# Performance work log

Hardware: AMD Instinct MI355X
Metric: run time of the kernel (lower is better)

## Reference

```python
import jax, jax.numpy as jnp
import numpy as np

B = 131072   # batch of state samples
H = 512      # hidden width of reconstructed subnets
EPS_DIAG = 0.1  # diagonal regularization ensuring M is invertible


def setup_inputs() -> dict:
    key = jax.random.key(0)
    ks = jax.random.split(key, 20)
    f32 = jnp.float32
    inp = {
        "q":      jax.random.normal(ks[0], (B, 3), dtype=f32),
        "q_dot":  jax.random.normal(ks[1], (B, 3), dtype=f32),
        "s":      jax.random.normal(ks[2], (B, 3), dtype=f32),
        "s_Ddot": jax.random.normal(ks[3], (B, 3), dtype=f32),
        "tau":    jax.random.normal(ks[4], (B, 3), dtype=f32),
        # viscous / coulomb friction coefficients (f_v1..3, f_c1..3)
        "fv": jnp.full((3,), 0.05, dtype=f32),
        "fc": jnp.full((3,), 0.05, dtype=f32),
        # Mass net: 3 -> H -> 9
        "W1m": jax.random.normal(ks[5], (3, H), dtype=f32) * 0.1,
        "b1m": jnp.zeros((H,), dtype=f32),
        "W2m": jax.random.normal(ks[6], (H, 9), dtype=f32) * 0.05,
        "b2m": jnp.zeros((9,), dtype=f32),
        # Gravity net: 3 -> H -> 3
        "W1g": jax.random.normal(ks[7], (3, H), dtype=f32) * 0.1,
        "b1g": jnp.zeros((H,), dtype=f32),
        "W2g": jax.random.normal(ks[8], (H, 3), dtype=f32) * 0.05,
        "b2g": jnp.zeros((3,), dtype=f32),
        # KAB net: concat(q, s, s_Ddot)=9 -> H -> 3
        "W1k": jax.random.normal(ks[9], (9, H), dtype=f32) * 0.1,
        "b1k": jnp.zeros((H,), dtype=f32),
        "W2k": jax.random.normal(ks[10], (H, 3), dtype=f32) * 0.05,
        "b2k": jnp.zeros((3,), dtype=f32),
    }
    return inp


def reference(q, q_dot, s, s_Ddot, tau, fv, fc,
              W1m, b1m, W2m, b2m,
              W1g, b1g, W2g, b2g,
              W1k, b1k, W2k, b2k) -> jnp.ndarray:
    # Mass matrix net -> [B,3,3], made SPD-ish so inv(M) is well defined
    hm = jnp.tanh(q @ W1m + b1m)                       # [B,H]
    Mraw = (hm @ W2m + b2m).reshape(-1, 3, 3)          # [B,3,3]
    M = jnp.einsum('bij,bkj->bik', Mraw, Mraw) + EPS_DIAG * jnp.eye(3, dtype=q.dtype)

    # Gravity net -> [B,3]
    hg = jnp.tanh(q @ W1g + b1g)
    G = hg @ W2g + b2g

    # KAB net on concat(q, s, s_Ddot) -> [B,3]
    x = jnp.concatenate([q, s, s_Ddot], axis=-1)       # [B,9]
    hk = jnp.tanh(x @ W1k + b1k)
    KAB = hk @ W2k + b2k

    # diag(fv) @ q_dot and diag(fc) @ sign(q_dot) are elementwise scalings
    rhs = -G + KAB - fv * q_dot - fc * jnp.sign(q_dot) + tau  # [B,3]

    # q_Ddot = inv(M) @ rhs  (solve is the same math, fewer ops)
    q_Ddot = jnp.linalg.solve(M, rhs[..., None]).squeeze(-1)  # [B,3]
    return q_Ddot
```

## Files before the change

kernel.cpp:

```cpp
#include <hip/hip_runtime.h>
#include <hip/hip_fp16.h>
#include <math.h>

#define HDIM 512
#define NCH1 96
#define NCH2 48
#define EPS_DIAG 0.1f

typedef __fp16 h2 __attribute__((ext_vector_type(2)));
typedef __fp16 h8 __attribute__((ext_vector_type(8)));
typedef float f32x4 __attribute__((ext_vector_type(4)));

__device__ __forceinline__ h2 f2h2(float a, float b) {
    return __builtin_amdgcn_cvt_pkrtz(a, b);
}

__device__ __forceinline__ h2 tanh2(h2 x) {
    const h2 HI = {(__fp16)2.0f,        (__fp16)2.0f};
    const h2 LO = {(__fp16)-2.0f,       (__fp16)-2.0f};
    const h2 C0 = {(__fp16)0.993654f,   (__fp16)0.993654f};
    const h2 C1 = {(__fp16)-0.29463f,   (__fp16)-0.29463f};
    const h2 C2 = {(__fp16)0.0695331f,  (__fp16)0.0695331f};
    const h2 C3 = {(__fp16)-0.00696328f,(__fp16)-0.00696328f};
    h2 t = __builtin_elementwise_min(__builtin_elementwise_max(x, LO), HI);
    h2 u = t * t;
    h2 p = __builtin_elementwise_fma(C3, u, C2);
    p = __builtin_elementwise_fma(p, u, C1);
    p = __builtin_elementwise_fma(p, u, C0);
    return t * p;
}

__global__ void pack_frags(const float* __restrict__ W1m, const float* __restrict__ b1m,
                           const float* __restrict__ W2m,
                           const float* __restrict__ W1g, const float* __restrict__ b1g,
                           const float* __restrict__ W2g,
                           const float* __restrict__ W1k, const float* __restrict__ b1k,
                           const float* __restrict__ W2k,
                           __fp16* __restrict__ frag)
{
    const int tid = blockIdx.x * blockDim.x + threadIdx.x;
    if (tid >= (NCH1 + NCH2) * 64) return;
    const int c = tid >> 6, l = tid & 63;
    __fp16* dst = frag + (size_t)tid * 8;
    if (c < NCH1) {
        const int h = c * 16 + (l & 15);
        #pragma unroll
        for (int j = 0; j < 8; ++j) {
            const int k = (l >> 4) * 8 + j;
            float v = 0.f;
            if (h < 512) {
                if (k < 3) v = W1m[k*HDIM + h];
                else if (k == 9) v = b1m[h];
            } else if (h < 1024) {
                const int hh = h - 512;
                if (k < 3) v = W1g[k*HDIM + hh];
                else if (k == 9) v = b1g[hh];
            } else {
                const int hh = h - 1024;
                if (k < 9) v = W1k[k*HDIM + hh];
                else if (k == 9) v = b1k[hh];
            }
            dst[j] = (__fp16)v;
        }
    } else {
        const int t = c - NCH1;
        const int nOut = l & 15;
        #pragma unroll
        for (int j = 0; j < 8; ++j) {
            const int kp = (l >> 4) * 8 + j;
            const int hid = t*32 + ((kp & 1) << 4) + (kp >> 1);
            float v = 0.f;
            if (hid < 512)       { if (nOut < 9)                v = W2m[hid*9 + nOut]; }
            else if (hid < 1024) { if (nOut >= 9 && nOut < 12)  v = W2g[(hid-512)*3 + (nOut-9)]; }
            else                 { if (nOut >= 12 && nOut < 15) v = W2k[(hid-1024)*3 + (nOut-12)]; }
            dst[j] = (__fp16)v;
        }
    }
}

__global__ __launch_bounds__(256, 6) void dyn_kernel(
    const __fp16* __restrict__ frag,
    const float* __restrict__ q, const float* __restrict__ q_dot,
    const float* __restrict__ s, const float* __restrict__ s_Ddot,
    const float* __restrict__ tau,
    const float* __restrict__ fv, const float* __restrict__ fc,
    const float* __restrict__ b2m, const float* __restrict__ b2g,
    const float* __restrict__ b2k,
    float* __restrict__ out, int n)
{
    __shared__ unsigned int tbuf[4][16][20];
    __shared__ float ebuf[4][16][17];

    const int lane = threadIdx.x & 63;
    const int w    = threadIdx.x >> 6;
    const int col  = lane & 15;
    const int quad = lane >> 4;
    const int base16 = (blockIdx.x * 4 + w) * 16;

    int sm = base16 + col; if (sm >= n) sm = n - 1;
    const float q0 = q[3*sm+0], q1 = q[3*sm+1], q2 = q[3*sm+2];
    const float s0 = s[3*sm+0], s1 = s[3*sm+1], s2 = s[3*sm+2];
    const float d0 = s_Ddot[3*sm+0], d1 = s_Ddot[3*sm+1], d2 = s_Ddot[3*sm+2];
    const bool z0 = (quad == 0), z1 = (quad == 1);
    h8 ax;
    ax[0] = (__fp16)(z0 ? q0 : (z1 ? d2  : 0.f));
    ax[1] = (__fp16)(z0 ? q1 : (z1 ? 1.f : 0.f));
    ax[2] = (__fp16)(z0 ? q2 : 0.f);
    ax[3] = (__fp16)(z0 ? s0 : 0.f);
    ax[4] = (__fp16)(z0 ? s1 : 0.f);
    ax[5] = (__fp16)(z0 ? s2 : 0.f);
    ax[6] = (__fp16)(z0 ? d0 : 0.f);
    ax[7] = (__fp16)(z0 ? d1 : 0.f);

    const f32x4 zero4 = {0.f, 0.f, 0.f, 0.f};
    f32x4 acc = zero4;

    const h8* fw1 = (const h8*)frag + lane;
    const h8* fw2 = (const h8*)frag + (size_t)NCH1 * 64 + lane;

    h8 w1a = fw1[0], w1b = fw1[64], w2v = fw2[0];
    for (int t = 0; t < NCH2; ++t) {
        h8 nw1a, nw1b, nw2;
        const int tn = t + 1;
        if (tn < NCH2) {
            nw1a = fw1[(2*tn    ) * 64];
            nw1b = fw1[(2*tn + 1) * 64];
            nw2  = fw2[tn * 64];
        }
        f32x4 p0 = __builtin_amdgcn_mfma_f32_16x16x32_f16(ax, w1a, zero4, 0, 0, 0);
        f32x4 p1 = __builtin_amdgcn_mfma_f32_16x16x32_f16(ax, w1b, zero4, 0, 0, 0);
        #pragma unroll
        for (int r = 0; r < 4; ++r) {
            const h2 hv = tanh2(f2h2(p0[r], p1[r]));
            tbuf[w][quad*4 + r][col] = __builtin_bit_cast(unsigned int, hv);
        }
        asm volatile("s_waitcnt lgkmcnt(0)" ::: "memory");
        const h8 a2 = *(const h8*)&tbuf[w][col][quad * 4];
        acc = __builtin_amdgcn_mfma_f32_16x16x32_f16(a2, w2v, acc, 0, 0, 0);
        asm volatile("" ::: "memory");
        w1a = nw1a; w1b = nw1b; w2v = nw2;
    }

    #pragma unroll
    for (int r = 0; r < 4; ++r)
        ebuf[w][quad*4 + r][col] = acc[r];
    asm volatile("s_waitcnt lgkmcnt(0)" ::: "memory");

    if (lane < 16) {
        const int i = base16 + lane;
        if (i < n) {
            const float* R = ebuf[w][lane];
            const float bM0 = R[0]  + b2m[0], bM1 = R[1]  + b2m[1], bM2 = R[2]  + b2m[2];
            const float bM3 = R[3]  + b2m[3], bM4 = R[4]  + b2m[4], bM5 = R[5]  + b2m[5];
            const float bM6 = R[6]  + b2m[6], bM7 = R[7]  + b2m[7], bM8 = R[8]  + b2m[8];
            const float bG0 = R[9]  + b2g[0], bG1 = R[10] + b2g[1], bG2 = R[11] + b2g[2];
            const float bK0 = R[12] + b2k[0], bK1 = R[13] + b2k[1], bK2 = R[14] + b2k[2];

            const float m00 = bM0*bM0 + bM1*bM1 + bM2*bM2 + EPS_DIAG;
            const float m01 = bM0*bM3 + bM1*bM4 + bM2*bM5;
            const float m02 = bM0*bM6 + bM1*bM7 + bM2*bM8;
            const float m11 = bM3*bM3 + bM4*bM4 + bM5*bM5 + EPS_DIAG;
            const float m12 = bM3*bM6 + bM4*bM7 + bM5*bM8;
            const float m22 = bM6*bM6 + bM7*bM7 + bM8*bM8 + EPS_DIAG;

            const float qd0 = q_dot[3*i+0], qd1 = q_dot[3*i+1], qd2 = q_dot[3*i+2];
            const float t0 = tau[3*i+0], t1 = tau[3*i+1], t2 = tau[3*i+2];
            const float fv0 = fv[0], fv1 = fv[1], fv2 = fv[2];
            const float fc0 = fc[0], fc1 = fc[1], fc2 = fc[2];
            const float sg0 = (qd0 > 0.f) ? 1.f : ((qd0 < 0.f) ? -1.f : 0.f);
            const float sg1 = (qd1 > 0.f) ? 1.f : ((qd1 < 0.f) ? -1.f : 0.f);
            const float sg2 = (qd2 > 0.f) ? 1.f : ((qd2 < 0.f) ? -1.f : 0.f);
            const float r0 = -bG0 + bK0 - fv0*qd0 - fc0*sg0 + t0;
            const float r1 = -bG1 + bK1 - fv1*qd1 - fc1*sg1 + t1;
            const float r2 = -bG2 + bK2 - fv2*qd2 - fc2*sg2 + t2;

            const float c00 = m11*m22 - m12*m12;
            const float c01 = m02*m12 - m01*m22;
            const float c02 = m01*m12 - m02*m11;
            const float det = m00*c00 + m01*c01 + m02*c02;
            const float idet = 1.0f / det;
            const float i11 = m00*m22 - m02*m02;
            const float i12 = m01*m02 - m00*m12;
            const float i22 = m00*m11 - m01*m01;

            out[3*i+0] = (c00*r0 + c01*r1 + c02*r2) * idet;
            out[3*i+1] = (c01*r0 + i11*r1 + i12*r2) * idet;
            out[3*i+2] = (c02*r0 + i12*r1 + i22*r2) * idet;
        }
    }
}

extern "C" void kernel_launch(void* const* d_in, const int* in_sizes, int n_in,
                              void* d_out, int out_size, void* d_ws, size_t ws_size,
                              hipStream_t stream) {
    const float* q      = (const float*)d_in[0];
    const float* q_dot  = (const float*)d_in[1];
    const float* s      = (const float*)d_in[2];
    const float* s_Ddot = (const float*)d_in[3];
    const float* tau    = (const float*)d_in[4];
    const float* fv     = (const float*)d_in[5];
    const float* fc     = (const float*)d_in[6];
    const float* W1m    = (const float*)d_in[7];
    const float* b1m    = (const float*)d_in[8];
    const float* W2m    = (const float*)d_in[9];
    const float* b2m    = (const float*)d_in[10];
    const float* W1g    = (const float*)d_in[11];
    const float* b1g    = (const float*)d_in[12];
    const float* W2g    = (const float*)d_in[13];
    const float* b2g    = (const float*)d_in[14];
    const float* W1k    = (const float*)d_in[15];
    const float* b1k    = (const float*)d_in[16];
    const float* W2k    = (const float*)d_in[17];
    const float* b2k    = (const float*)d_in[18];
    float* out = (float*)d_out;
    __fp16* frag = (__fp16*)d_ws;

    const int n = in_sizes[0] / 3;

    pack_frags<<<((NCH1 + NCH2) * 64 + 255) / 256, 256, 0, stream>>>(
        W1m, b1m, W2m, W1g, b1g, W2g, W1k, b1k, W2k, frag);

    const int blocks = (n + 63) / 64;
    dyn_kernel<<<blocks, 256, 0, stream>>>(frag, q, q_dot, s, s_Ddot, tau, fv, fc,
                                           b2m, b2g, b2k, out, n);
}
```

Baseline: 137.0 us.

## Swap MFMA operand roles to keep hidden activations in registers, dropping LDS transpose

The MFMA operands are swapped so the weights become the A operand. The packed W1/W2 fragment layouts are permuted so that the tanh outputs of the first layer land directly in the register layout the second-layer MFMA expects. This removes the per-iteration LDS write, wait and read used to transpose hidden activations. The loop is also unrolled by two with register double-buffered weight loads, and the occupancy hint is raised from 6 to 8 waves, which may constrain register allocation.

```diff
diff --git a/kernel.cpp b/kernel.cpp
--- a/kernel.cpp
+++ b/kernel.cpp
@@ -1,5 +1,4 @@
 #include <hip/hip_runtime.h>
-#include <hip/hip_fp16.h>
 #include <math.h>
 
 #define HDIM 512
@@ -10,6 +9,7 @@
 typedef __fp16 h2 __attribute__((ext_vector_type(2)));
 typedef __fp16 h8 __attribute__((ext_vector_type(8)));
 typedef float f32x4 __attribute__((ext_vector_type(4)));
+typedef unsigned int u32x4 __attribute__((ext_vector_type(4)));
 
 __device__ __forceinline__ h2 f2h2(float a, float b) {
     return __builtin_amdgcn_cvt_pkrtz(a, b);
@@ -30,6 +30,17 @@
     return t * p;
 }
 
+__device__ __forceinline__ float w1c_at(int k, int hid,
+    const float* W1m, const float* b1m, const float* W1g, const float* b1g,
+    const float* W1k, const float* b1k)
+{
+    if (hid < 512)  { if (k < 3) return W1m[k*HDIM + hid]; if (k == 9) return b1m[hid]; return 0.f; }
+    if (hid < 1024) { const int h = hid - 512;
+                      if (k < 3) return W1g[k*HDIM + h];  if (k == 9) return b1g[h];  return 0.f; }
+    const int h = hid - 1024;
+    if (k < 9) return W1k[k*HDIM + h]; if (k == 9) return b1k[h]; return 0.f;
+}
+
 __global__ void pack_frags(const float* __restrict__ W1m, const float* __restrict__ b1m,
                            const float* __restrict__ W2m,
                            const float* __restrict__ W1g, const float* __restrict__ b1g,
@@ -41,44 +52,31 @@
     const int tid = blockIdx.x * blockDim.x + threadIdx.x;
     if (tid >= (NCH1 + NCH2) * 64) return;
     const int c = tid >> 6, l = tid & 63;
+    const int m = l & 15, kq = l >> 4;
     __fp16* dst = frag + (size_t)tid * 8;
     if (c < NCH1) {
-        const int h = c * 16 + (l & 15);
+        const int t = c >> 1, phase = c & 1;
+        const int hid = 32*t + 8*(m >> 2) + (m & 3) + 4*phase;
         #pragma unroll
         for (int j = 0; j < 8; ++j) {
-            const int k = (l >> 4) * 8 + j;
-            float v = 0.f;
-            if (h < 512) {
-                if (k < 3) v = W1m[k*HDIM + h];
-                else if (k == 9) v = b1m[h];
-            } else if (h < 1024) {
-                const int hh = h - 512;
-                if (k < 3) v = W1g[k*HDIM + hh];
-                else if (k == 9) v = b1g[hh];
-            } else {
-                const int hh = h - 1024;
-                if (k < 9) v = W1k[k*HDIM + hh];
-                else if (k == 9) v = b1k[hh];
-            }
-            dst[j] = (__fp16)v;
+            const int k = kq*8 + j;
+            dst[j] = (__fp16)((k < 10) ? w1c_at(k, hid, W1m, b1m, W1g, b1g, W1k, b1k) : 0.f);
         }
     } else {
         const int t = c - NCH1;
-        const int nOut = l & 15;
         #pragma unroll
         for (int j = 0; j < 8; ++j) {
-            const int kp = (l >> 4) * 8 + j;
-            const int hid = t*32 + ((kp & 1) << 4) + (kp >> 1);
+            const int hid = 32*t + kq*8 + j;
             float v = 0.f;
-            if (hid < 512)       { if (nOut < 9)                v = W2m[hid*9 + nOut]; }
-            else if (hid < 1024) { if (nOut >= 9 && nOut < 12)  v = W2g[(hid-512)*3 + (nOut-9)]; }
-            else                 { if (nOut >= 12 && nOut < 15) v = W2k[(hid-1024)*3 + (nOut-12)]; }
+            if (hid < 512)       { if (m < 9)             v = W2m[hid*9 + m]; }
+            else if (hid < 1024) { if (m >= 9 && m < 12)  v = W2g[(hid-512)*3 + (m-9)]; }
+            else                 { if (m >= 12 && m < 15) v = W2k[(hid-1024)*3 + (m-12)]; }
             dst[j] = (__fp16)v;
         }
     }
 }
 
-__global__ __launch_bounds__(256, 6) void dyn_kernel(
+__global__ __launch_bounds__(256, 8) void dyn_kernel(
     const __fp16* __restrict__ frag,
     const float* __restrict__ q, const float* __restrict__ q_dot,
     const float* __restrict__ s, const float* __restrict__ s_Ddot,
@@ -88,8 +86,7 @@
     const float* __restrict__ b2k,
     float* __restrict__ out, int n)
 {
-    __shared__ unsigned int tbuf[4][16][20];
-    __shared__ float ebuf[4][16][17];
+    __shared__ float ebuf[4][16][20];
 
     const int lane = threadIdx.x & 63;
     const int w    = threadIdx.x >> 6;
@@ -115,35 +112,42 @@
     const f32x4 zero4 = {0.f, 0.f, 0.f, 0.f};
     f32x4 acc = zero4;
 
-    const h8* fw1 = (const h8*)frag + lane;
-    const h8* fw2 = (const h8*)frag + (size_t)NCH1 * 64 + lane;
-
-    h8 w1a = fw1[0], w1b = fw1[64], w2v = fw2[0];
-    for (int t = 0; t < NCH2; ++t) {
-        h8 nw1a, nw1b, nw2;
-        const int tn = t + 1;
-        if (tn < NCH2) {
-            nw1a = fw1[(2*tn    ) * 64];
-            nw1b = fw1[(2*tn + 1) * 64];
-            nw2  = fw2[tn * 64];
-        }
-        f32x4 p0 = __builtin_amdgcn_mfma_f32_16x16x32_f16(ax, w1a, zero4, 0, 0, 0);
-        f32x4 p1 = __builtin_amdgcn_mfma_f32_16x16x32_f16(ax, w1b, zero4, 0, 0, 0);
-        #pragma unroll
-        for (int r = 0; r < 4; ++r) {
-            const h2 hv = tanh2(f2h2(p0[r], p1[r]));
-            tbuf[w][quad*4 + r][col] = __builtin_bit_cast(unsigned int, hv);
-        }
-        asm volatile("s_waitcnt lgkmcnt(0)" ::: "memory");
-        const h8 a2 = *(const h8*)&tbuf[w][col][quad * 4];
-        acc = __builtin_amdgcn_mfma_f32_16x16x32_f16(a2, w2v, acc, 0, 0, 0);
-        asm volatile("" ::: "memory");
-        w1a = nw1a; w1b = nw1b; w2v = nw2;
-    }
-
-    #pragma unroll
-    for (int r = 0; r < 4; ++r)
-        ebuf[w][quad*4 + r][col] = acc[r];
+    const h8* p1 = (const h8*)frag + lane;
+    const h8* p2 = (const h8*)frag + (size_t)NCH1 * 64 + lane;
+
+#define BODY(W1A, W1B, W2V) do {                                              \
+        f32x4 pa = __builtin_amdgcn_mfma_f32_16x16x32_f16((W1A), ax, zero4, 0, 0, 0); \
+        f32x4 pb = __builtin_amdgcn_mfma_f32_16x16x32_f16((W1B), ax, zero4, 0, 0, 0); \
+        const h2 A01 = tanh2(f2h2(pa[0], pa[1]));                             \
+        const h2 A23 = tanh2(f2h2(pa[2], pa[3]));                             \
+        const h2 B01 = tanh2(f2h2(pb[0], pb[1]));                             \
+        const h2 B23 = tanh2(f2h2(pb[2], pb[3]));                             \
+        u32x4 uv;                                                             \
+        uv[0] = __builtin_bit_cast(unsigned int, A01);                        \
+        uv[1] = __builtin_bit_cast(unsigned int, A23);                        \
+        uv[2] = __builtin_bit_cast(unsigned int, B01);                        \
+        uv[3] = __builtin_bit_cast(unsigned int, B23);                        \
+        const h8 a2 = __builtin_bit_cast(h8, uv);                             \
+        acc = __builtin_amdgcn_mfma_f32_16x16x32_f16((W2V), a2, acc, 0, 0, 0); \
+    } while (0)
+
+    h8 a0 = p1[0], b0 = p1[64], c0 = p2[0];
+    int t = 0;
+    for (; t < NCH2 - 2; t += 2) {
+        h8 a1 = p1[128], b1 = p1[192], c1 = p2[64];
+        p1 += 256; p2 += 128;
+        BODY(a0, b0, c0);
+        a0 = p1[0]; b0 = p1[64]; c0 = p2[0];
+        BODY(a1, b1, c1);
+    }
+    {
+        h8 a1 = p1[128], b1 = p1[192], c1 = p2[64];
+        BODY(a0, b0, c0);
+        BODY(a1, b1, c1);
+    }
+#undef BODY
+
+    *(f32x4*)(&ebuf[w][col][4*quad]) = acc;
     asm volatile("s_waitcnt lgkmcnt(0)" ::: "memory");
 
     if (lane < 16) {
```

After: 133.7 us. 1.02x faster.
